# Kernel tuning notes

Measured on AMD Instinct MI355X. Metric: run time of the kernel, lower is better.

## Reference

```python
import jax, jax.numpy as jnp
import numpy as np

D = 1024       # d_model
DFF = 4 * D    # MLP hidden
L = 8          # n_layers
V = 32000      # vocab
B, S = 4, 2048
EPS = 1e-5


def sinusoidal_pe(seq_len, d_model, dtype=jnp.float32):
    pos = jnp.arange(seq_len, dtype=jnp.float32)[:, None]            # [S,1]
    div = jnp.exp(jnp.arange(0, d_model, 2, dtype=jnp.float32) * (-np.log(10000.0) / d_model))  # [D/2]
    pe = jnp.zeros((seq_len, d_model), dtype=jnp.float32)
    pe = pe.at[:, 0::2].set(jnp.sin(pos * div))
    pe = pe.at[:, 1::2].set(jnp.cos(pos * div))
    return pe.astype(dtype)


def layer_norm(x, g, b):
    mu = jnp.mean(x, axis=-1, keepdims=True)
    var = jnp.mean(jnp.square(x - mu), axis=-1, keepdims=True)
    return (x - mu) * jax.lax.rsqrt(var + EPS) * g + b


def setup_inputs() -> dict:
    key = jax.random.key(0)
    ks = jax.random.split(key, 12)
    sd = 0.02
    tokens = jax.random.randint(ks[0], (B, S), 0, V, dtype=jnp.int32)
    emb = jax.random.normal(ks[1], (V, D), dtype=jnp.float32) * sd
    Wq = jax.random.normal(ks[2], (L, D, D), dtype=jnp.float32) * sd
    Wk = jax.random.normal(ks[3], (L, D, D), dtype=jnp.float32) * sd
    Wv = jax.random.normal(ks[4], (L, D, D), dtype=jnp.float32) * sd
    bq = jnp.zeros((L, D), jnp.float32)
    bk = jnp.zeros((L, D), jnp.float32)
    bv = jnp.zeros((L, D), jnp.float32)
    g1 = jnp.ones((L, D), jnp.float32)
    beta1 = jnp.zeros((L, D), jnp.float32)
    g2 = jnp.ones((L, D), jnp.float32)
    beta2 = jnp.zeros((L, D), jnp.float32)
    W1 = jax.random.normal(ks[5], (L, D, DFF), dtype=jnp.float32) * sd
    bm1 = jnp.zeros((L, DFF), jnp.float32)
    W2 = jax.random.normal(ks[6], (L, DFF, D), dtype=jnp.float32) * sd
    bm2 = jnp.zeros((L, D), jnp.float32)
    return dict(tokens=tokens, emb=emb, Wq=Wq, bq=bq, Wk=Wk, bk=bk, Wv=Wv, bv=bv,
                g1=g1, beta1=beta1, g2=g2, beta2=beta2, W1=W1, bm1=bm1, W2=W2, bm2=bm2)


def reference(tokens, emb, Wq, bq, Wk, bk, Wv, bv, g1, beta1, g2, beta2, W1, bm1, W2, bm2):
    x = emb[tokens]                                  # [B,S,D]
    x = x + sinusoidal_pe(x.shape[1], D)[None]
    scale = jnp.sqrt(jnp.asarray(D, x.dtype))
    for i in range(L):
        h = layer_norm(x, g1[i], beta1[i])
        q = h @ Wq[i] + bq[i]
        k = h @ Wk[i] + bk[i]
        v = h @ Wv[i] + bv[i]
        scores = jnp.einsum('bsd,btd->bst', q, k) / scale   # [B,S,S]
        attn = jax.nn.softmax(scores, axis=-1)
        x = x + jnp.einsum('bst,btd->bsd', attn, v)
        h2 = layer_norm(x, g2[i], beta2[i])
        x = x + (jax.nn.relu(h2 @ W1[i] + bm1[i]) @ W2[i] + bm2[i])
    return x
```

## Files before the change

### kernel.cpp

```cpp
#include <hip/hip_runtime.h>
#include <cstdint>

typedef __bf16 bf16_t;
typedef bf16_t bf16x8 __attribute__((ext_vector_type(8)));
typedef float f32x4 __attribute__((ext_vector_type(4)));

#define D_MODEL 1024
#define DFF_    4096
#define NLAYER  8
#define BB      4
#define SS      2048
#define MS      (BB*SS)

__device__ __forceinline__ void gload_lds16(const void* g, void* l) {
  typedef __attribute__((address_space(1))) void gv_t;
  typedef __attribute__((address_space(3))) void lv_t;
  __builtin_amdgcn_global_load_lds((gv_t*)(uintptr_t)g, (lv_t*)(uintptr_t)l, 16, 0, 0);
}

__global__ __launch_bounds__(256) void embed_pe_kernel(
    const int* __restrict__ tokens, const float* __restrict__ emb,
    float* __restrict__ x) {
  int idx = blockIdx.x * 256 + threadIdx.x;
  int d  = idx & (D_MODEL - 1);
  int bs = idx >> 10;
  int s  = bs & (SS - 1);
  int tok = tokens[bs];
  float e = emb[(size_t)tok * D_MODEL + d];
  int i2 = d & ~1;
  float div = __expf((float)i2 * (-9.210340371976184f / (float)D_MODEL));
  float ang = (float)s * div;
  float pe = (d & 1) ? cosf(ang) : sinf(ang);
  x[idx] = e + pe;
}

__global__ __launch_bounds__(256) void ln_kernel(
    const float* __restrict__ xin, const float* __restrict__ g,
    const float* __restrict__ beta, bf16_t* __restrict__ out) {
  const size_t row = blockIdx.x;
  const int t = threadIdx.x;
  const float* xr = xin + row * D_MODEL;
  float4 vx = ((const float4*)xr)[t];
  float s = vx.x + vx.y + vx.z + vx.w;
#pragma unroll
  for (int o = 32; o > 0; o >>= 1) s += __shfl_down(s, o);
  __shared__ float red[8];
  const int lane = t & 63, w = t >> 6;
  if (lane == 0) red[w] = s;
  __syncthreads();
  const float mu = (red[0] + red[1] + red[2] + red[3]) * (1.f / D_MODEL);
  float d0 = vx.x - mu, d1 = vx.y - mu, d2 = vx.z - mu, d3 = vx.w - mu;
  float sq = d0 * d0 + d1 * d1 + d2 * d2 + d3 * d3;
#pragma unroll
  for (int o = 32; o > 0; o >>= 1) sq += __shfl_down(sq, o);
  if (lane == 0) red[4 + w] = sq;
  __syncthreads();
  const float var = (red[4] + red[5] + red[6] + red[7]) * (1.f / D_MODEL);
  const float rs = rsqrtf(var + 1e-5f);
  float4 gg = ((const float4*)g)[t];
  float4 bb = ((const float4*)beta)[t];
  alignas(8) bf16_t o4[4];
  o4[0] = (bf16_t)(d0 * rs * gg.x + bb.x);
  o4[1] = (bf16_t)(d1 * rs * gg.y + bb.y);
  o4[2] = (bf16_t)(d2 * rs * gg.z + bb.z);
  o4[3] = (bf16_t)(d3 * rs * gg.w + bb.w);
  *(uint2*)&out[row * D_MODEL + t * 4] = *(const uint2*)o4;
}

__global__ __launch_bounds__(256) void softmax_kernel(
    const float* __restrict__ sc, bf16_t* __restrict__ attn) {
  const size_t row = blockIdx.x;
  const int t = threadIdx.x;
  const float* sr = sc + row * SS;
  float4 a = ((const float4*)sr)[t];
  float4 b = ((const float4*)sr)[t + 256];
  const float scl = 0.03125f;
  float v[8] = {a.x * scl, a.y * scl, a.z * scl, a.w * scl,
                b.x * scl, b.y * scl, b.z * scl, b.w * scl};
  float mx = v[0];
#pragma unroll
  for (int j = 1; j < 8; ++j) mx = fmaxf(mx, v[j]);
#pragma unroll
  for (int o = 32; o > 0; o >>= 1) mx = fmaxf(mx, __shfl_down(mx, o));
  __shared__ float red[8];
  const int lane = t & 63, w = t >> 6;
  if (lane == 0) red[w] = mx;
  __syncthreads();
  mx = fmaxf(fmaxf(red[0], red[1]), fmaxf(red[2], red[3]));
  float p[8];
  float sum = 0.f;
#pragma unroll
  for (int j = 0; j < 8; ++j) { p[j] = __expf(v[j] - mx); sum += p[j]; }
#pragma unroll
  for (int o = 32; o > 0; o >>= 1) sum += __shfl_down(sum, o);
  if (lane == 0) red[4 + w] = sum;
  __syncthreads();
  const float inv = 1.f / (red[4] + red[5] + red[6] + red[7]);
  alignas(16) bf16_t o8[8];
#pragma unroll
  for (int j = 0; j < 8; ++j) o8[j] = (bf16_t)(p[j] * inv);
  bf16_t* outp = attn + row * SS;
  *(uint2*)&outp[t * 4]        = *(const uint2*)&o8[0];
  *(uint2*)&outp[1024 + t * 4] = *(const uint2*)&o8[4];
}

template <typename TI>
__global__ __launch_bounds__(256) void transpose_cast_kernel(
    const TI* __restrict__ src, bf16_t* __restrict__ dst, int R, int C) {
  __shared__ bf16_t tile[32][33];
  const int bx = blockIdx.x * 32, by = blockIdx.y * 32;
  const size_t off = (size_t)blockIdx.z * (size_t)R * (size_t)C;
  const int tx = threadIdx.x & 31, ty4 = threadIdx.x >> 5;
#pragma unroll
  for (int j = 0; j < 4; ++j) {
    int a = ty4 * 4 + j;
    tile[a][tx] = (bf16_t)(float)src[off + (size_t)(by + a) * C + bx + tx];
  }
  __syncthreads();
#pragma unroll
  for (int j = 0; j < 4; ++j) {
    int b = ty4 * 4 + j;
    dst[off + (size_t)(bx + b) * R + by + tx] = tile[tx][b];
  }
}

template <bool BIAS, bool RELU, bool RES, typename OUT_T>
__global__ __launch_bounds__(256) void gemm_nt(
    const bf16_t* __restrict__ A, const bf16_t* __restrict__ Bt,
    OUT_T* __restrict__ C, const float* __restrict__ bias,
    const float* __restrict__ res, int K, int lda, int ldb, int ldc,
    long long strideA, long long strideB, long long strideC) {
  __shared__ bf16_t As[128 * 32];
  __shared__ bf16_t Bs[128 * 32];
  const int tid = threadIdx.x;
  const int lane = tid & 63;
  const int wv = tid >> 6;
  const int wm = wv & 1, wn = wv >> 1;
  const long long z = blockIdx.z;
  A += z * strideA;
  Bt += z * strideB;
  C += z * strideC;
  const float* resp = RES ? (res + z * strideC) : nullptr;
  const int m0 = blockIdx.y * 128, n0 = blockIdx.x * 128;

  f32x4 acc[4][4];
#pragma unroll
  for (int i = 0; i < 4; ++i)
#pragma unroll
    for (int j = 0; j < 4; ++j) acc[i][j] = (f32x4){0.f, 0.f, 0.f, 0.f};

  const int arow = tid >> 2;
  const int acol = (tid & 3) * 8;
  const int lm = lane & 15, quad = lane >> 4;
  const int nK = K >> 5;
  for (int kb = 0; kb < nK; ++kb) {
    const int k0 = kb * 32;
    gload_lds16(A + (size_t)(m0 + arow) * lda + k0 + acol, &As[(size_t)tid * 8]);
    gload_lds16(A + (size_t)(m0 + arow + 64) * lda + k0 + acol, &As[(size_t)(tid + 256) * 8]);
    gload_lds16(Bt + (size_t)(n0 + arow) * ldb + k0 + acol, &Bs[(size_t)tid * 8]);
    gload_lds16(Bt + (size_t)(n0 + arow + 64) * ldb + k0 + acol, &Bs[(size_t)(tid + 256) * 8]);
    __syncthreads();
    bf16x8 af[4], bfv[4];
#pragma unroll
    for (int mt = 0; mt < 4; ++mt)
      af[mt] = *(const bf16x8*)&As[(wm * 64 + mt * 16 + lm) * 32 + quad * 8];
#pragma unroll
    for (int nt = 0; nt < 4; ++nt)
      bfv[nt] = *(const bf16x8*)&Bs[(wn * 64 + nt * 16 + lm) * 32 + quad * 8];
#pragma unroll
    for (int mt = 0; mt < 4; ++mt)
#pragma unroll
      for (int nt = 0; nt < 4; ++nt)
        acc[mt][nt] = __builtin_amdgcn_mfma_f32_16x16x32_bf16(af[mt], bfv[nt], acc[mt][nt], 0, 0, 0);
    __syncthreads();
  }
#pragma unroll
  for (int mt = 0; mt < 4; ++mt) {
#pragma unroll
    for (int nt = 0; nt < 4; ++nt) {
      const int col = n0 + wn * 64 + nt * 16 + lm;
      float bv = 0.f;
      if (BIAS) bv = bias[col];
#pragma unroll
      for (int r = 0; r < 4; ++r) {
        const int row = m0 + wm * 64 + mt * 16 + quad * 4 + r;
        float val = acc[mt][nt][r] + bv;
        if (RES) val += resp[(size_t)row * ldc + col];
        if (RELU) val = fmaxf(val, 0.f);
        C[(size_t)row * ldc + col] = (OUT_T)val;
      }
    }
  }
}

extern "C" void kernel_launch(void* const* d_in, const int* in_sizes, int n_in,
                              void* d_out, int out_size, void* d_ws, size_t ws_size,
                              hipStream_t stream) {
  const int*   tokens = (const int*)d_in[0];
  const float* emb    = (const float*)d_in[1];
  const float* Wq     = (const float*)d_in[2];
  const float* bq     = (const float*)d_in[3];
  const float* Wk     = (const float*)d_in[4];
  const float* bk     = (const float*)d_in[5];
  const float* Wv     = (const float*)d_in[6];
  const float* bv     = (const float*)d_in[7];
  const float* g1     = (const float*)d_in[8];
  const float* beta1  = (const float*)d_in[9];
  const float* g2     = (const float*)d_in[10];
  const float* beta2  = (const float*)d_in[11];
  const float* W1     = (const float*)d_in[12];
  const float* bm1    = (const float*)d_in[13];
  const float* W2     = (const float*)d_in[14];
  const float* bm2    = (const float*)d_in[15];

  char* wp = (char*)d_ws;
  auto carve = [&](size_t bytes) -> void* {
    void* p = (void*)wp;
    wp += (bytes + 255) & ~(size_t)255;
    return p;
  };
  bf16_t* WqT  = (bf16_t*)carve((size_t)D_MODEL * D_MODEL * 2);
  bf16_t* WkT  = (bf16_t*)carve((size_t)D_MODEL * D_MODEL * 2);
  bf16_t* WvT  = (bf16_t*)carve((size_t)D_MODEL * D_MODEL * 2);
  bf16_t* W1T  = (bf16_t*)carve((size_t)D_MODEL * DFF_ * 2);
  bf16_t* W2T  = (bf16_t*)carve((size_t)D_MODEL * DFF_ * 2);
  float*  x    = (float*)carve((size_t)MS * D_MODEL * 4);
  bf16_t* h    = (bf16_t*)carve((size_t)MS * D_MODEL * 2);
  bf16_t* q    = (bf16_t*)carve((size_t)MS * D_MODEL * 2);
  bf16_t* kbuf = (bf16_t*)carve((size_t)MS * D_MODEL * 2);
  bf16_t* vbuf = (bf16_t*)carve((size_t)MS * D_MODEL * 2);
  float*  sc   = (float*)carve((size_t)BB * SS * SS * 4);
  bf16_t* attn = (bf16_t*)carve((size_t)BB * SS * SS * 2);
  bf16_t* vT   = q;
  bf16_t* mbuf = (bf16_t*)sc;

  embed_pe_kernel<<<(MS * D_MODEL) / 256, 256, 0, stream>>>(tokens, emb, x);

  for (int i = 0; i < NLAYER; ++i) {
    const size_t wOff  = (size_t)i * D_MODEL * D_MODEL;
    const size_t w1Off = (size_t)i * D_MODEL * DFF_;
    transpose_cast_kernel<float><<<dim3(32, 32, 1), 256, 0, stream>>>(Wq + wOff, WqT, D_MODEL, D_MODEL);
    transpose_cast_kernel<float><<<dim3(32, 32, 1), 256, 0, stream>>>(Wk + wOff, WkT, D_MODEL, D_MODEL);
    transpose_cast_kernel<float><<<dim3(32, 32, 1), 256, 0, stream>>>(Wv + wOff, WvT, D_MODEL, D_MODEL);
    transpose_cast_kernel<float><<<dim3(128, 32, 1), 256, 0, stream>>>(W1 + w1Off, W1T, D_MODEL, DFF_);
    transpose_cast_kernel<float><<<dim3(32, 128, 1), 256, 0, stream>>>(W2 + w1Off, W2T, DFF_, D_MODEL);

    ln_kernel<<<MS, 256, 0, stream>>>(x, g1 + i * D_MODEL, beta1 + i * D_MODEL, h);

    gemm_nt<true, false, false, bf16_t><<<dim3(8, 64, 1), 256, 0, stream>>>(
        h, WqT, q, bq + i * D_MODEL, nullptr, D_MODEL, D_MODEL, D_MODEL, D_MODEL, 0, 0, 0);
    gemm_nt<true, false, false, bf16_t><<<dim3(8, 64, 1), 256, 0, stream>>>(
        h, WkT, kbuf, bk + i * D_MODEL, nullptr, D_MODEL, D_MODEL, D_MODEL, D_MODEL, 0, 0, 0);
    gemm_nt<true, false, false, bf16_t><<<dim3(8, 64, 1), 256, 0, stream>>>(
        h, WvT, vbuf, bv + i * D_MODEL, nullptr, D_MODEL, D_MODEL, D_MODEL, D_MODEL, 0, 0, 0);

    gemm_nt<false, false, false, float><<<dim3(16, 16, BB), 256, 0, stream>>>(
        q, kbuf, sc, nullptr, nullptr, D_MODEL, D_MODEL, D_MODEL, SS,
        (long long)SS * D_MODEL, (long long)SS * D_MODEL, (long long)SS * SS);

    softmax_kernel<<<BB * SS, 256, 0, stream>>>(sc, attn);

    transpose_cast_kernel<bf16_t><<<dim3(32, 64, BB), 256, 0, stream>>>(vbuf, vT, SS, D_MODEL);

    gemm_nt<false, false, true, float><<<dim3(8, 16, BB), 256, 0, stream>>>(
        attn, vT, x, nullptr, x, SS, SS, SS, D_MODEL,
        (long long)SS * SS, (long long)D_MODEL * SS, (long long)SS * D_MODEL);

    ln_kernel<<<MS, 256, 0, stream>>>(x, g2 + i * D_MODEL, beta2 + i * D_MODEL, h);

    gemm_nt<true, true, false, bf16_t><<<dim3(32, 64, 1), 256, 0, stream>>>(
        h, W1T, mbuf, bm1 + i * DFF_, nullptr, D_MODEL, D_MODEL, D_MODEL, DFF_, 0, 0, 0);

    float* outC = (i == NLAYER - 1) ? (float*)d_out : x;
    gemm_nt<true, false, true, float><<<dim3(8, 64, 1), 256, 0, stream>>>(
        mbuf, W2T, outC, bm2 + i * D_MODEL, x, DFF_, DFF_, DFF_, D_MODEL, 0, 0, 0);
  }
}
```

Measured before the change: 4.250 ms.

## Fuse QKV projections, deepen GEMM K-tile with swizzled LDS, add grouped tile rasterization

Merges the three Q/K/V projection GEMMs into one GEMM against a packed [3072x1024] weight with packed biases, writing a strided qkv buffer that the score and transpose kernels read directly. The GEMM K-step grows from 32 to 64, halving the barrier count per tile, and LDS rows are XOR-swizzled to avoid bank conflicts. Blocks are remapped with grouped-M rasterization plus an XCD-aware interleave to improve L2 reuse. This adds larger LDS use per block, which may lower occupancy, and index arithmetic in every block.

```diff
diff --git a/kernel.cpp b/kernel.cpp
--- a/kernel.cpp
+++ b/kernel.cpp
@@ -104,23 +104,38 @@
   *(uint2*)&outp[1024 + t * 4] = *(const uint2*)&o8[4];
 }
 
+__global__ __launch_bounds__(256) void pack_bias_kernel(
+    const float* __restrict__ bq, const float* __restrict__ bk,
+    const float* __restrict__ bv, float* __restrict__ out) {
+  const int l = blockIdx.x;
+#pragma unroll
+  for (int j = 0; j < 4; ++j) {
+    int t = j * 256 + threadIdx.x;
+    out[l * 3072 + t]        = bq[l * 1024 + t];
+    out[l * 3072 + 1024 + t] = bk[l * 1024 + t];
+    out[l * 3072 + 2048 + t] = bv[l * 1024 + t];
+  }
+}
+
 template <typename TI>
 __global__ __launch_bounds__(256) void transpose_cast_kernel(
-    const TI* __restrict__ src, bf16_t* __restrict__ dst, int R, int C) {
+    const TI* __restrict__ src, bf16_t* __restrict__ dst, int C,
+    int ldS, int ldD, long long srcZ, long long dstZ) {
   __shared__ bf16_t tile[32][33];
   const int bx = blockIdx.x * 32, by = blockIdx.y * 32;
-  const size_t off = (size_t)blockIdx.z * (size_t)R * (size_t)C;
+  const size_t soff = (size_t)blockIdx.z * (size_t)srcZ;
+  const size_t doff = (size_t)blockIdx.z * (size_t)dstZ;
   const int tx = threadIdx.x & 31, ty4 = threadIdx.x >> 5;
 #pragma unroll
   for (int j = 0; j < 4; ++j) {
     int a = ty4 * 4 + j;
-    tile[a][tx] = (bf16_t)(float)src[off + (size_t)(by + a) * C + bx + tx];
+    tile[a][tx] = (bf16_t)(float)src[soff + (size_t)(by + a) * ldS + bx + tx];
   }
   __syncthreads();
 #pragma unroll
   for (int j = 0; j < 4; ++j) {
     int b = ty4 * 4 + j;
-    dst[off + (size_t)(bx + b) * R + by + tx] = tile[tx][b];
+    dst[doff + (size_t)(bx + b) * ldD + by + tx] = tile[tx][b];
   }
 }
 
@@ -129,19 +144,31 @@
     const bf16_t* __restrict__ A, const bf16_t* __restrict__ Bt,
     OUT_T* __restrict__ C, const float* __restrict__ bias,
     const float* __restrict__ res, int K, int lda, int ldb, int ldc,
+    int nm, int nn,
     long long strideA, long long strideB, long long strideC) {
-  __shared__ bf16_t As[128 * 32];
-  __shared__ bf16_t Bs[128 * 32];
+  __shared__ bf16_t As[128 * 64];
+  __shared__ bf16_t Bs[128 * 64];
   const int tid = threadIdx.x;
   const int lane = tid & 63;
   const int wv = tid >> 6;
   const int wm = wv & 1, wn = wv >> 1;
-  const long long z = blockIdx.z;
+  const long long z = blockIdx.y;
   A += z * strideA;
   Bt += z * strideB;
   C += z * strideC;
   const float* resp = RES ? (res + z * strideC) : nullptr;
-  const int m0 = blockIdx.y * 128, n0 = blockIdx.x * 128;
+
+  int id = blockIdx.x;
+  const int T = nm * nn;
+  if ((T & 7) == 0) id = (id & 7) * (T >> 3) + (id >> 3);
+  const int GM = 8;
+  const int g = id / (GM * nn);
+  const int fm = g * GM;
+  const int gsz = (nm - fm < GM) ? (nm - fm) : GM;
+  const int lid = id - g * (GM * nn);
+  const int pm = fm + (lid % gsz);
+  const int pn = lid / gsz;
+  const int m0 = pm * 128, n0 = pn * 128;
 
   f32x4 acc[4][4];
 #pragma unroll
@@ -149,29 +176,46 @@
 #pragma unroll
     for (int j = 0; j < 4; ++j) acc[i][j] = (f32x4){0.f, 0.f, 0.f, 0.f};
 
-  const int arow = tid >> 2;
-  const int acol = (tid & 3) * 8;
   const int lm = lane & 15, quad = lane >> 4;
-  const int nK = K >> 5;
+  const int srow = tid >> 3;
+  const int schk = tid & 7;
+  const int nK = K >> 6;
   for (int kb = 0; kb < nK; ++kb) {
-    const int k0 = kb * 32;
-    gload_lds16(A + (size_t)(m0 + arow) * lda + k0 + acol, &As[(size_t)tid * 8]);
-    gload_lds16(A + (size_t)(m0 + arow + 64) * lda + k0 + acol, &As[(size_t)(tid + 256) * 8]);
-    gload_lds16(Bt + (size_t)(n0 + arow) * ldb + k0 + acol, &Bs[(size_t)tid * 8]);
-    gload_lds16(Bt + (size_t)(n0 + arow + 64) * ldb + k0 + acol, &Bs[(size_t)(tid + 256) * 8]);
+    const int k0 = kb << 6;
+#pragma unroll
+    for (int p = 0; p < 4; ++p) {
+      const int r = p * 32 + srow;
+      const int cg = schk ^ (r & 7);
+      gload_lds16(A + (size_t)(m0 + r) * lda + k0 + cg * 8, &As[(size_t)(p * 256 + tid) * 8]);
+    }
+#pragma unroll
+    for (int p = 0; p < 4; ++p) {
+      const int r = p * 32 + srow;
+      const int cg = schk ^ (r & 7);
+      gload_lds16(Bt + (size_t)(n0 + r) * ldb + k0 + cg * 8, &Bs[(size_t)(p * 256 + tid) * 8]);
+    }
     __syncthreads();
-    bf16x8 af[4], bfv[4];
-#pragma unroll
-    for (int mt = 0; mt < 4; ++mt)
-      af[mt] = *(const bf16x8*)&As[(wm * 64 + mt * 16 + lm) * 32 + quad * 8];
-#pragma unroll
-    for (int nt = 0; nt < 4; ++nt)
-      bfv[nt] = *(const bf16x8*)&Bs[(wn * 64 + nt * 16 + lm) * 32 + quad * 8];
-#pragma unroll
-    for (int mt = 0; mt < 4; ++mt)
-#pragma unroll
-      for (int nt = 0; nt < 4; ++nt)
-        acc[mt][nt] = __builtin_amdgcn_mfma_f32_16x16x32_bf16(af[mt], bfv[nt], acc[mt][nt], 0, 0, 0);
+#pragma unroll
+    for (int kk = 0; kk < 2; ++kk) {
+      bf16x8 af[4], bfv[4];
+#pragma unroll
+      for (int mt = 0; mt < 4; ++mt) {
+        const int r = wm * 64 + mt * 16 + lm;
+        const int c = (kk * 4 + quad) ^ (r & 7);
+        af[mt] = *(const bf16x8*)&As[r * 64 + c * 8];
+      }
+#pragma unroll
+      for (int nt = 0; nt < 4; ++nt) {
+        const int r = wn * 64 + nt * 16 + lm;
+        const int c = (kk * 4 + quad) ^ (r & 7);
+        bfv[nt] = *(const bf16x8*)&Bs[r * 64 + c * 8];
+      }
+#pragma unroll
+      for (int mt = 0; mt < 4; ++mt)
+#pragma unroll
+        for (int nt = 0; nt < 4; ++nt)
+          acc[mt][nt] = __builtin_amdgcn_mfma_f32_16x16x32_bf16(af[mt], bfv[nt], acc[mt][nt], 0, 0, 0);
+    }
     __syncthreads();
   }
 #pragma unroll
@@ -219,60 +263,63 @@
     wp += (bytes + 255) & ~(size_t)255;
     return p;
   };
-  bf16_t* WqT  = (bf16_t*)carve((size_t)D_MODEL * D_MODEL * 2);
-  bf16_t* WkT  = (bf16_t*)carve((size_t)D_MODEL * D_MODEL * 2);
-  bf16_t* WvT  = (bf16_t*)carve((size_t)D_MODEL * D_MODEL * 2);
-  bf16_t* W1T  = (bf16_t*)carve((size_t)D_MODEL * DFF_ * 2);
-  bf16_t* W2T  = (bf16_t*)carve((size_t)D_MODEL * DFF_ * 2);
-  float*  x    = (float*)carve((size_t)MS * D_MODEL * 4);
-  bf16_t* h    = (bf16_t*)carve((size_t)MS * D_MODEL * 2);
-  bf16_t* q    = (bf16_t*)carve((size_t)MS * D_MODEL * 2);
-  bf16_t* kbuf = (bf16_t*)carve((size_t)MS * D_MODEL * 2);
-  bf16_t* vbuf = (bf16_t*)carve((size_t)MS * D_MODEL * 2);
-  float*  sc   = (float*)carve((size_t)BB * SS * SS * 4);
-  bf16_t* attn = (bf16_t*)carve((size_t)BB * SS * SS * 2);
-  bf16_t* vT   = q;
-  bf16_t* mbuf = (bf16_t*)sc;
+  bf16_t* WqkvT = (bf16_t*)carve((size_t)3 * D_MODEL * D_MODEL * 2);
+  bf16_t* W1T   = (bf16_t*)carve((size_t)D_MODEL * DFF_ * 2);
+  bf16_t* W2T   = (bf16_t*)carve((size_t)D_MODEL * DFF_ * 2);
+  float*  bqkv  = (float*)carve((size_t)NLAYER * 3072 * 4);
+  float*  x     = (float*)carve((size_t)MS * D_MODEL * 4);
+  bf16_t* h     = (bf16_t*)carve((size_t)MS * D_MODEL * 2);
+  bf16_t* qkv   = (bf16_t*)carve((size_t)MS * 3072 * 2);
+  float*  sc    = (float*)carve((size_t)BB * SS * SS * 4);
+  bf16_t* attn  = (bf16_t*)carve((size_t)BB * SS * SS * 2);
+  bf16_t* vT    = h;
+  bf16_t* mbuf  = (bf16_t*)sc;
 
   embed_pe_kernel<<<(MS * D_MODEL) / 256, 256, 0, stream>>>(tokens, emb, x);
+  pack_bias_kernel<<<NLAYER, 256, 0, stream>>>(bq, bk, bv, bqkv);
 
   for (int i = 0; i < NLAYER; ++i) {
     const size_t wOff  = (size_t)i * D_MODEL * D_MODEL;
     const size_t w1Off = (size_t)i * D_MODEL * DFF_;
-    transpose_cast_kernel<float><<<dim3(32, 32, 1), 256, 0, stream>>>(Wq + wOff, WqT, D_MODEL, D_MODEL);
-    transpose_cast_kernel<float><<<dim3(32, 32, 1), 256, 0, stream>>>(Wk + wOff, WkT, D_MODEL, D_MODEL);
-    transpose_cast_kernel<float><<<dim3(32, 32, 1), 256, 0, stream>>>(Wv + wOff, WvT, D_MODEL, D_MODEL);
-    transpose_cast_kernel<float><<<dim3(128, 32, 1), 256, 0, stream>>>(W1 + w1Off, W1T, D_MODEL, DFF_);
-    transpose_cast_kernel<float><<<dim3(32, 128, 1), 256, 0, stream>>>(W2 + w1Off, W2T, DFF_, D_MODEL);
+    transpose_cast_kernel<float><<<dim3(32, 32, 1), 256, 0, stream>>>(
+        Wq + wOff, WqkvT, D_MODEL, D_MODEL, D_MODEL, 0, 0);
+    transpose_cast_kernel<float><<<dim3(32, 32, 1), 256, 0, stream>>>(
+        Wk + wOff, WqkvT + (size_t)1024 * D_MODEL, D_MODEL, D_MODEL, D_MODEL, 0, 0);
+    transpose_cast_kernel<float><<<dim3(32, 32, 1), 256, 0, stream>>>(
+        Wv + wOff, WqkvT + (size_t)2048 * D_MODEL, D_MODEL, D_MODEL, D_MODEL, 0, 0);
+    transpose_cast_kernel<float><<<dim3(128, 32, 1), 256, 0, stream>>>(
+        W1 + w1Off, W1T, DFF_, DFF_, D_MODEL, 0, 0);
+    transpose_cast_kernel<float><<<dim3(32, 128, 1), 256, 0, stream>>>(
+        W2 + w1Off, W2T, D_MODEL, D_MODEL, DFF_, 0, 0);
 
     ln_kernel<<<MS, 256, 0, stream>>>(x, g1 + i * D_MODEL, beta1 + i * D_MODEL, h);
 
-    gemm_nt<true, false, false, bf16_t><<<dim3(8, 64, 1), 256, 0, stream>>>(
-        h, WqT, q, bq + i * D_MODEL, nullptr, D_MODEL, D_MODEL, D_MODEL, D_MODEL, 0, 0, 0);
-    gemm_nt<true, false, false, bf16_t><<<dim3(8, 64, 1), 256, 0, stream>>>(
-        h, WkT, kbuf, bk + i * D_MODEL, nullptr, D_MODEL, D_MODEL, D_MODEL, D_MODEL, 0, 0, 0);
-    gemm_nt<true, false, false, bf16_t><<<dim3(8, 64, 1), 256, 0, stream>>>(
-        h, WvT, vbuf, bv + i * D_MODEL, nullptr, D_MODEL, D_MODEL, D_MODEL, D_MODEL, 0, 0, 0);
-
-    gemm_nt<false, false, false, float><<<dim3(16, 16, BB), 256, 0, stream>>>(
-        q, kbuf, sc, nullptr, nullptr, D_MODEL, D_MODEL, D_MODEL, SS,
-        (long long)SS * D_MODEL, (long long)SS * D_MODEL, (long long)SS * SS);
+    gemm_nt<true, false, false, bf16_t><<<dim3(64 * 24, 1), 256, 0, stream>>>(
+        h, WqkvT, qkv, bqkv + i * 3072, nullptr, D_MODEL, D_MODEL, D_MODEL, 3072,
+        64, 24, 0, 0, 0);
+
+    gemm_nt<false, false, false, float><<<dim3(256, BB), 256, 0, stream>>>(
+        qkv, qkv + 1024, sc, nullptr, nullptr, D_MODEL, 3072, 3072, SS,
+        16, 16, (long long)SS * 3072, (long long)SS * 3072, (long long)SS * SS);
 
     softmax_kernel<<<BB * SS, 256, 0, stream>>>(sc, attn);
 
-    transpose_cast_kernel<bf16_t><<<dim3(32, 64, BB), 256, 0, stream>>>(vbuf, vT, SS, D_MODEL);
-
-    gemm_nt<false, false, true, float><<<dim3(8, 16, BB), 256, 0, stream>>>(
+    transpose_cast_kernel<bf16_t><<<dim3(32, 64, BB), 256, 0, stream>>>(
+        qkv + 2048, vT, D_MODEL, 3072, SS, (long long)SS * 3072, (long long)D_MODEL * SS);
+
+    gemm_nt<false, false, true, float><<<dim3(128, BB), 256, 0, stream>>>(
         attn, vT, x, nullptr, x, SS, SS, SS, D_MODEL,
-        (long long)SS * SS, (long long)D_MODEL * SS, (long long)SS * D_MODEL);
+        16, 8, (long long)SS * SS, (long long)D_MODEL * SS, (long long)SS * D_MODEL);
 
     ln_kernel<<<MS, 256, 0, stream>>>(x, g2 + i * D_MODEL, beta2 + i * D_MODEL, h);
 
-    gemm_nt<true, true, false, bf16_t><<<dim3(32, 64, 1), 256, 0, stream>>>(
-        h, W1T, mbuf, bm1 + i * DFF_, nullptr, D_MODEL, D_MODEL, D_MODEL, DFF_, 0, 0, 0);
+    gemm_nt<true, true, false, bf16_t><<<dim3(64 * 32, 1), 256, 0, stream>>>(
+        h, W1T, mbuf, bm1 + i * DFF_, nullptr, D_MODEL, D_MODEL, D_MODEL, DFF_,
+        64, 32, 0, 0, 0);
 
     float* outC = (i == NLAYER - 1) ? (float*)d_out : x;
-    gemm_nt<true, false, true, float><<<dim3(8, 64, 1), 256, 0, stream>>>(
-        mbuf, W2T, outC, bm2 + i * D_MODEL, x, DFF_, DFF_, DFF_, D_MODEL, 0, 0, 0);
-  }
-}
+    gemm_nt<true, false, true, float><<<dim3(64 * 8, 1), 256, 0, stream>>>(
+        mbuf, W2T, outC, bm2 + i * D_MODEL, x, DFF_, DFF_, DFF_, D_MODEL,
+        64, 8, 0, 0, 0);
+  }
+}
```

New measurement: 3.485 ms. 18.0% less time.
